# Optimization experiments

Measured on AMD Instinct MI355X. Metric: run time of the kernel, lower is better.

## Reference

```python
import jax, jax.numpy as jnp
import numpy as np

GROUPS = 32
EPS = 1e-5


def _group_norm(x, w, b):
    B, C, H, W = x.shape
    xr = x.reshape(B, GROUPS, C // GROUPS, H, W)
    mean = xr.mean(axis=(2, 3, 4), keepdims=True)
    var = xr.var(axis=(2, 3, 4), keepdims=True)
    xn = ((xr - mean) * jax.lax.rsqrt(var + EPS)).reshape(B, C, H, W)
    return xn * w[None, :, None, None] + b[None, :, None, None]


def _conv1x1(w, b, x):
    # 1x1 conv == per-pixel channel matmul
    return jnp.einsum('oc,bchw->bohw', w, x) + b[None, :, None, None]


def setup_inputs() -> dict:
    key = jax.random.key(0)
    ks = jax.random.split(key, 6)
    C = 512
    s = 1.0 / np.sqrt(C)  # kaiming-uniform-ish scale for 1x1 convs
    return {
        'x': jax.random.normal(ks[0], (4, C, 64, 64), jnp.float32),
        'gn_w': jnp.ones((C,), jnp.float32),
        'gn_b': jnp.zeros((C,), jnp.float32),
        'qw': jax.random.normal(ks[1], (C, C), jnp.float32) * s,
        'qb': jnp.zeros((C,), jnp.float32),
        'kw': jax.random.normal(ks[2], (C, C), jnp.float32) * s,
        'kb': jnp.zeros((C,), jnp.float32),
        'vw': jax.random.normal(ks[3], (C, C), jnp.float32) * s,
        'vb': jnp.zeros((C,), jnp.float32),
        'pw': jax.random.normal(ks[4], (C, C), jnp.float32) * s,
        'pb': jnp.zeros((C,), jnp.float32),
    }


def reference(x, gn_w, gn_b, qw, qb, kw, kb, vw, vb, pw, pb):
    B, C, H, W = x.shape
    h_ = _group_norm(x, gn_w, gn_b)
    q = _conv1x1(qw, qb, h_).reshape(B, C, H * W)
    k = _conv1x1(kw, kb, h_).reshape(B, C, H * W)
    v = _conv1x1(vw, vb, h_).reshape(B, C, H * W)
    # scores [B, HW(query), HW(key)]
    scores = jnp.einsum('bcq,bck->bqk', q, k) * (C ** -0.5)
    attn = jax.nn.softmax(scores, axis=-1)
    out = jnp.einsum('bqk,bdk->bdq', attn, v).reshape(B, C, H, W)
    return x + _conv1x1(pw, pb, out)
```

## Files before the change

kernel.cpp:

```cpp
#include <hip/hip_runtime.h>

#define DEV __device__ __forceinline__

typedef __attribute__((ext_vector_type(8))) short short8;
typedef __attribute__((ext_vector_type(4))) float floatx4;
typedef __attribute__((ext_vector_type(4))) int i32x4;
typedef __attribute__((ext_vector_type(2))) long longx2;

DEV unsigned short f2bs(float x) {
    unsigned u = __float_as_uint(x);
    unsigned r = (u + 0x7fffu + ((u >> 16) & 1u)) >> 16;
    return (unsigned short)r;
}

DEV unsigned char f2fp8(float x) {
#if __has_builtin(__builtin_amdgcn_cvt_pk_fp8_f32)
    int pk = __builtin_amdgcn_cvt_pk_fp8_f32(x, 0.f, 0, false);
    return (unsigned char)(pk & 0xff);
#else
    unsigned u = __float_as_uint(x);
    unsigned s = (u >> 24) & 0x80;
    unsigned a = u & 0x7fffffff;
    unsigned um = a + 0x7ffffu + ((a >> 20) & 1u);
    unsigned r = (a >= 0x3c800000u) ? ((um >> 20) - 0x3C0u) : 0u;
    return (unsigned char)(r | s);
#endif
}

DEV unsigned pack_fp8x4(float v0, float v1, float v2, float v3) {
#if __has_builtin(__builtin_amdgcn_cvt_pk_fp8_f32)
    unsigned pk = (unsigned)__builtin_amdgcn_cvt_pk_fp8_f32(v0, v1, 0, false);
    pk = (unsigned)__builtin_amdgcn_cvt_pk_fp8_f32(v2, v3, (int)pk, true);
    return pk;
#else
    return (unsigned)f2fp8(v0) | ((unsigned)f2fp8(v1) << 8) |
           ((unsigned)f2fp8(v2) << 16) | ((unsigned)f2fp8(v3) << 24);
#endif
}

DEV unsigned pack_i8x4(float v0, float v1, float v2, float v3) {
    unsigned b0 = (unsigned)((int)rintf(v0)) & 255u;
    unsigned b1 = (unsigned)((int)rintf(v1)) & 255u;
    unsigned b2 = (unsigned)((int)rintf(v2)) & 255u;
    unsigned b3 = (unsigned)((int)rintf(v3)) & 255u;
    return b0 | (b1 << 8) | (b2 << 16) | (b3 << 24);
}

DEV void syncfull() {
    asm volatile("s_waitcnt vmcnt(0) lgkmcnt(0)" ::: "memory");
    __builtin_amdgcn_sched_barrier(0);
    __builtin_amdgcn_s_barrier();
    __builtin_amdgcn_sched_barrier(0);
}

__global__ void pre_kernel(const float* __restrict__ x,
                           const float* __restrict__ qw, const float* __restrict__ kw,
                           const float* __restrict__ vw, const float* __restrict__ pw,
                           const float* __restrict__ qb, const float* __restrict__ kb,
                           unsigned short* __restrict__ wqkb, unsigned short* __restrict__ wvb,
                           unsigned short* __restrict__ wpb,
                           float* __restrict__ biasqk,
                           float* __restrict__ stats) {
    int b = blockIdx.x, tid = threadIdx.x;
    if (b < 768) {
        const float* src = (b < 256) ? qw : (b < 512) ? kw : vw;
        unsigned short* dst = (b < 256) ? wqkb : (b < 512) ? (wqkb + 262144) : wvb;
        int off = (b & 255) * 256 + tid;
        float4 v = ((const float4*)src)[off];
        ushort4 o;
        o.x = f2bs(v.x); o.y = f2bs(v.y); o.z = f2bs(v.z); o.w = f2bs(v.w);
        ((ushort4*)dst)[off] = o;
    } else if (b < 1024) {
        int off = (b - 768) * 256 + tid;
        int row = off >> 7, c4 = (off & 127) * 4;
        float4 v = ((const float4*)pw)[off];
        float vv[4] = {v.x, v.y, v.z, v.w};
#pragma unroll
        for (int e = 0; e < 4; ++e) {
            int c = c4 + e;
            int j = (c >> 4) & 3, lc = c & 15;
            int cp = (c & ~63) | (lc * 4 + j);
            wpb[row * 512 + cp] = f2bs(vv[e]);
        }
    } else if (b == 1024) {
        biasqk[tid]       = qb[tid];
        biasqk[256 + tid] = qb[256 + tid];
        biasqk[512 + tid] = kb[tid];
        biasqk[768 + tid] = kb[256 + tid];
    } else {
        int bg = b - 1025;
        const float4* p = (const float4*)(x + (size_t)bg * 65536);
        float s = 0.f, ss = 0.f;
        for (int i = tid; i < 16384; i += 256) {
            float4 v = p[i];
            s += v.x + v.y + v.z + v.w;
            ss += v.x * v.x + v.y * v.y + v.z * v.z + v.w * v.w;
        }
        for (int off = 32; off; off >>= 1) { s += __shfl_down(s, off); ss += __shfl_down(ss, off); }
        __shared__ float rs[4], rss[4];
        int wave = tid >> 6, lane = tid & 63;
        if (lane == 0) { rs[wave] = s; rss[wave] = ss; }
        __syncthreads();
        if (tid == 0) {
            float S = rs[0] + rs[1] + rs[2] + rs[3];
            float SS = rss[0] + rss[1] + rss[2] + rss[3];
            float mean = S * (1.f / 65536.f);
            float var = SS * (1.f / 65536.f) - mean * mean;
            stats[bg * 2] = mean;
            stats[bg * 2 + 1] = rsqrtf(var + 1e-5f);
        }
    }
}

__global__ void gn_apply_kernel(const float* __restrict__ x, const float* __restrict__ stats,
                                const float* __restrict__ gw, const float* __restrict__ gb,
                                unsigned short* __restrict__ ht) {
    __shared__ __align__(16) unsigned short t[64][72];
    int b = blockIdx.z, c0 = blockIdx.y * 64, p0 = blockIdx.x * 64;
    int tid = threadIdx.x;
    const float* xb = x + ((size_t)b * 512 + c0) * 4096 + p0;
#pragma unroll
    for (int pass = 0; pass < 4; ++pass) {
        int cl = pass * 16 + (tid >> 4);
        int pq = (tid & 15) * 4;
        float4 v = *(const float4*)(xb + (size_t)cl * 4096 + pq);
        int c = c0 + cl, g = c >> 4;
        float mean = stats[(b * 32 + g) * 2], rstd = stats[(b * 32 + g) * 2 + 1];
        float sw = gw[c] * rstd;
        float sb = gb[c] - mean * sw;
        t[pq + 0][cl] = f2bs(v.x * sw + sb);
        t[pq + 1][cl] = f2bs(v.y * sw + sb);
        t[pq + 2][cl] = f2bs(v.z * sw + sb);
        t[pq + 3][cl] = f2bs(v.w * sw + sb);
    }
    __syncthreads();
    unsigned short* hb = ht + ((size_t)b * 4096 + p0) * 512 + c0;
#pragma unroll
    for (int pass = 0; pass < 2; ++pass) {
        int pl = pass * 32 + (tid >> 3);
        int c8 = (tid & 7) * 8;
        *(uint4*)(hb + (size_t)pl * 512 + c8) = *(const uint4*)&t[pl][c8];
    }
}

__global__ void gemm_qkv(const unsigned short* __restrict__ h_t, long long sP,
                         const unsigned short* __restrict__ wqkb,
                         const unsigned short* __restrict__ wvb,
                         char* __restrict__ q_i8, char* __restrict__ k_i8,
                         char* __restrict__ v_f8,
                         const float* __restrict__ biasqk, const float* __restrict__ vb,
                         float qs) {
    __shared__ __align__(16) unsigned short lA[128 * 64];
    __shared__ __align__(16) unsigned short lB[128 * 64];
    const int tid = threadIdx.x;
    const int wave = tid >> 6, lane = tid & 63;
    const int flat = blockIdx.x;
    const bool isqk = flat < 1024;
    int m0, n0, bz;
    const unsigned short *Ab, *Bb;
    if (isqk) {
        m0 = ((flat >> 3) & 31) * 128;
        n0 = (flat & 7) * 128;
        bz = flat >> 8;
        Ab = h_t + (size_t)bz * sP;
        Bb = wqkb;
    } else {
        const int g = flat - 1024;
        m0 = ((g >> 5) & 3) * 128;
        n0 = (g & 31) * 128;
        bz = g >> 7;
        Ab = wvb;
        Bb = h_t + (size_t)bz * sP;
    }

    floatx4 acc[4][4];
#pragma unroll
    for (int i = 0; i < 4; i++)
#pragma unroll
        for (int j = 0; j < 4; j++) acc[i][j] = (floatx4){0.f, 0.f, 0.f, 0.f};

    const int wm = (wave >> 1) * 64, wn = (wave & 1) * 64;
    const int quad = lane >> 4;
    const int lc = lane & 15;
    const int lc7 = lc & 7;

    for (int kt = 0; kt < 8; ++kt) {
        const int kbase = kt * 64;
#pragma unroll
        for (int c = 0; c < 4; ++c) {
            int d = c * 256 + tid;
            int r = d >> 3;
            int kc = (d & 7) ^ (r & 7);
            const unsigned short* ga = Ab + (size_t)(m0 + r) * 512 + kbase + kc * 8;
            const unsigned short* gb = Bb + (size_t)(n0 + r) * 512 + kbase + kc * 8;
            __builtin_amdgcn_global_load_lds(
                (const __attribute__((address_space(1))) void*)ga,
                (__attribute__((address_space(3))) void*)&lA[(size_t)(c * 256 + wave * 64) * 8], 16, 0, 0);
            __builtin_amdgcn_global_load_lds(
                (const __attribute__((address_space(1))) void*)gb,
                (__attribute__((address_space(3))) void*)&lB[(size_t)(c * 256 + wave * 64) * 8], 16, 0, 0);
        }
        __syncthreads();
#pragma unroll
        for (int kk = 0; kk < 2; ++kk) {
            const int swz = ((kk * 4 + quad) ^ lc7) * 8;
            short8 af[4], bf[4];
#pragma unroll
            for (int i = 0; i < 4; i++)
                af[i] = *(const short8*)&lA[(size_t)(wm + i * 16 + lc) * 64 + swz];
#pragma unroll
            for (int j = 0; j < 4; j++)
                bf[j] = *(const short8*)&lB[(size_t)(wn + j * 16 + lc) * 64 + swz];
#pragma unroll
            for (int i = 0; i < 4; i++)
#pragma unroll
                for (int j = 0; j < 4; j++)
                    acc[i][j] = __builtin_amdgcn_mfma_f32_16x16x32_bf16(af[i], bf[j], acc[i][j], 0, 0, 0);
        }
        __syncthreads();
    }

    const int rowb = quad * 4;
    if (isqk) {
#pragma unroll
        for (int i = 0; i < 4; i++) {
#pragma unroll
            for (int r = 0; r < 4; r++) {
                const int m = m0 + wm + i * 16 + rowb + r;
                float q[4];
#pragma unroll
                for (int j = 0; j < 4; j++) {
                    const int n = n0 + wn + j * 16 + lc;
                    q[j] = fminf(fmaxf((acc[i][j][r] + biasqk[n]) * qs, -127.f), 127.f);
                }
                const int col64 = n0 + wn;
                char* outp = (col64 < 512) ? q_i8 : k_i8;
                size_t idx = (size_t)bz * sP + (size_t)m * 512 +
                             (col64 - ((col64 < 512) ? 0 : 512)) + lc * 4;
                *(unsigned*)(outp + idx) = pack_i8x4(q[0], q[1], q[2], q[3]);
            }
        }
    } else {
#pragma unroll
        for (int i = 0; i < 4; i++) {
#pragma unroll
            for (int r = 0; r < 4; r++) {
                const int m = m0 + wm + i * 16 + rowb + r;
                const float bm = vb[m];
                float q[4];
#pragma unroll
                for (int j = 0; j < 4; j++)
                    q[j] = fminf(fmaxf(acc[i][j][r] + bm, -448.f), 448.f);
                size_t idx = (size_t)bz * sP + (size_t)m * 4096 + n0 + wn + lc * 4;
                *(unsigned*)(v_f8 + idx) = pack_fp8x4(q[0], q[1], q[2], q[3]);
            }
        }
    }
}

__global__ void gemm_proj(const unsigned short* __restrict__ A,
                          const unsigned short* __restrict__ B, long long sBb,
                          float* __restrict__ Cv, long long sCb,
                          const float* __restrict__ bias,
                          const float* __restrict__ resid, long long sRb,
                          const float* __restrict__ rsum,
                          int M, int N, int K) {
    __shared__ __align__(16) unsigned short lA[128 * 64];
    __shared__ __align__(16) unsigned short lB[128 * 64];
    const int tid = threadIdx.x;
    const int wave = tid >> 6, lane = tid & 63;
    const int m0 = blockIdx.y * 128, n0 = blockIdx.x * 128, bz = blockIdx.z;
    const unsigned short* Ab = A;
    const unsigned short* Bb = B + (size_t)bz * sBb;

    floatx4 acc[4][4];
#pragma unroll
    for (int i = 0; i < 4; i++)
#pragma unroll
        for (int j = 0; j < 4; j++) acc[i][j] = (floatx4){0.f, 0.f, 0.f, 0.f};

    const int wm = (wave >> 1) * 64, wn = (wave & 1) * 64;
    const int quad = lane >> 4;
    const int lc = lane & 15;
    const int lc7 = lc & 7;

    const int nk = K >> 6;
    for (int kt = 0; kt < nk; ++kt) {
        const int kbase = kt * 64;
#pragma unroll
        for (int c = 0; c < 4; ++c) {
            int d = c * 256 + tid;
            int r = d >> 3;
            int kc = (d & 7) ^ (r & 7);
            const unsigned short* ga = Ab + (size_t)(m0 + r) * 512 + ((kbase & 511) + kc * 8);
            const unsigned short* gb = Bb + (size_t)(n0 + r) * 1024 + kbase + kc * 8;
            __builtin_amdgcn_global_load_lds(
                (const __attribute__((address_space(1))) void*)ga,
                (__attribute__((address_space(3))) void*)&lA[(size_t)(c * 256 + wave * 64) * 8], 16, 0, 0);
            __builtin_amdgcn_global_load_lds(
                (const __attribute__((address_space(1))) void*)gb,
                (__attribute__((address_space(3))) void*)&lB[(size_t)(c * 256 + wave * 64) * 8], 16, 0, 0);
        }
        __syncthreads();
#pragma unroll
        for (int kk = 0; kk < 2; ++kk) {
            const int swz = ((kk * 4 + quad) ^ lc7) * 8;
            short8 af[4], bf[4];
#pragma unroll
            for (int i = 0; i < 4; i++)
                af[i] = *(const short8*)&lA[(size_t)(wm + i * 16 + lc) * 64 + swz];
#pragma unroll
            for (int j = 0; j < 4; j++)
                bf[j] = *(const short8*)&lB[(size_t)(wn + j * 16 + lc) * 64 + swz];
#pragma unroll
            for (int i = 0; i < 4; i++)
#pragma unroll
                for (int j = 0; j < 4; j++)
                    acc[i][j] = __builtin_amdgcn_mfma_f32_16x16x32_bf16(af[i], bf[j], acc[i][j], 0, 0, 0);
        }
        __syncthreads();
    }

    float rsinv[4];
#pragma unroll
    for (int j = 0; j < 4; j++) {
        const int n = n0 + wn + j * 16 + lc;
        rsinv[j] = 1.f / (rsum[(size_t)bz * 4096 + n] + rsum[(size_t)(4 + bz) * 4096 + n]);
    }

    const int rowb = quad * 4;
#pragma unroll
    for (int i = 0; i < 4; i++) {
#pragma unroll
        for (int r = 0; r < 4; r++) {
            const int m = m0 + wm + i * 16 + rowb + r;
            const float bm = bias[m];
#pragma unroll
            for (int j = 0; j < 4; j++) {
                const int n = n0 + wn + j * 16 + lc;
                size_t idx = (size_t)bz * sCb + (size_t)m * N + n;
                Cv[idx] = acc[i][j][r] * rsinv[j] + bm + resid[(size_t)bz * sRb + (size_t)m * N + n];
            }
        }
    }
}

__global__ __launch_bounds__(512, 2) void attn_fused(
    const char* __restrict__ Qg, const char* __restrict__ Kg,
    const char* __restrict__ Vg,
    unsigned short* __restrict__ Ou, long long sOb,
    float* __restrict__ rsum, float scale2) {
    __shared__ __align__(16) char Ql[512 * 128];
    __shared__ __align__(16) char Kl[256 * 128];
    __shared__ __align__(16) char Vl[256 * 128];
    __shared__ __align__(16) char Pl[128 * 80];
    const int tid = threadIdx.x;
    const int wave = tid >> 6, lane = tid & 63;
    const int quad = lane >> 4, lc = lane & 15;
    const int lc7 = lc & 7;
    const int id = blockIdx.x;
    const int xcd = id & 7, qi = id >> 3;
    const int bz = xcd >> 1, split = xcd & 1;
    const int q0 = qi * 128;
    const int kvbase = split * 2048;
    const int NIT = 32;

    const char* Qb = Qg + ((size_t)bz * 4096 + q0) * 512;
    const char* Kb = Kg + ((size_t)bz * 4096 + kvbase) * 512;
    const char* Vb = Vg + (size_t)bz * 2097152 + kvbase;

    const int wq = wave * 16;
    const int mO = (wave >> 2) * 64, nO = (wave & 3) * 128;

    auto stageQ = [&]() {
#pragma unroll
        for (int c = 0; c < 8; ++c) {
            int f = c * 512 + tid;
            int rr = f >> 3, cs = f & 7;
            int qq = rr & 127, chq = rr >> 7;
            int s = cs ^ (qq & 7);
            __builtin_amdgcn_global_load_lds(
                (const __attribute__((address_space(1))) void*)(Qb + (size_t)qq * 512 + chq * 128 + s * 16),
                (__attribute__((address_space(3))) void*)(Ql + (size_t)f * 16), 16, 0, 0);
        }
    };
    auto stageK = [&](int t) {
#pragma unroll
        for (int c = 0; c < 4; ++c) {
            int f = c * 512 + tid;
            int rr = f >> 3, cs = f & 7;
            int kv = rr & 63, chq = rr >> 6;
            int s = cs ^ (kv & 7);
            __builtin_amdgcn_global_load_lds(
                (const __attribute__((address_space(1))) void*)(Kb + (size_t)(t * 64 + kv) * 512 + chq * 128 + s * 16),
                (__attribute__((address_space(3))) void*)(Kl + (size_t)f * 16), 16, 0, 0);
        }
    };
    auto stageV = [&](int t) {
#pragma unroll
        for (int c = 0; c < 4; ++c) {
            int f = c * 512 + tid;
            int rr = f >> 3, cs = f & 7;
            int cp = cs ^ (rr & 7);
            int d = rr + ((cp >> 2) << 8);
            int gq = cp & 3;
            __builtin_amdgcn_global_load_lds(
                (const __attribute__((address_space(1))) void*)(Vb + (size_t)d * 4096 + t * 64 + gq * 16),
                (__attribute__((address_space(3))) void*)(Vl + (size_t)f * 16), 16, 0, 0);
        }
    };

    floatx4 acco[4][8];
#pragma unroll
    for (int i = 0; i < 4; ++i)
#pragma unroll
        for (int j = 0; j < 8; ++j) acco[i][j] = (floatx4){0.f, 0.f, 0.f, 0.f};
    float rs = 0.f;

    stageQ();
    stageK(0);
    stageV(0);
    syncfull();

    const int q = wq + lc;
    const int q7 = q & 7;

    for (int t = 0; t < NIT; ++t) {
        if (t > 0) stageV(t);
        i32x4 accs[4];
#pragma unroll
        for (int ki = 0; ki < 4; ++ki) accs[ki] = (i32x4){0, 0, 0, 0};
#pragma unroll
        for (int ks = 0; ks < 8; ++ks) {
            const int g = ks * 4 + quad;
            const int gh = g >> 3, gl = g & 7;
            i32x4 bfrag = *(const i32x4*)&Ql[(size_t)(gh * 128 + q) * 128 + ((gl ^ q7) << 4)];
#pragma unroll
            for (int ki = 0; ki < 4; ++ki) {
                const int ar = ki * 16 + lc;
                i32x4 afrag = *(const i32x4*)&Kl[(size_t)(gh * 64 + ar) * 128 + ((gl ^ lc7) << 4)];
                accs[ki] = __builtin_amdgcn_mfma_i32_16x16x64_i8(afrag, bfrag, accs[ki], 0, 0, 0);
            }
        }
        float e[4][4];
#pragma unroll
        for (int ki = 0; ki < 4; ++ki)
#pragma unroll
            for (int r = 0; r < 4; ++r) {
                e[ki][r] = fminf(exp2f(fmaf((float)accs[ki][r], scale2, -2.0f)), 448.f);
                rs += e[ki][r];
            }
        {
            unsigned w0 = pack_fp8x4(e[0][0], e[1][0], e[2][0], e[3][0]);
            unsigned w1 = pack_fp8x4(e[0][1], e[1][1], e[2][1], e[3][1]);
            unsigned w2 = pack_fp8x4(e[0][2], e[1][2], e[2][2], e[3][2]);
            unsigned w3 = pack_fp8x4(e[0][3], e[1][3], e[2][3], e[3][3]);
            uint2 s0; s0.x = w0; s0.y = w1;
            uint2 s1; s1.x = w2; s1.y = w3;
            *(uint2*)&Pl[(size_t)q * 80 + quad * 16 + 0] = s0;
            *(uint2*)&Pl[(size_t)q * 80 + quad * 16 + 8] = s1;
        }
        syncfull();

        if (t + 1 < NIT) stageK(t + 1);
        {
            longx2 pv[4], vv[8];
#pragma unroll
            for (int i = 0; i < 4; ++i) {
                const int row = mO + i * 16 + lc;
                pv[i] = *(const longx2*)&Pl[(size_t)row * 80 + quad * 16];
            }
#pragma unroll
            for (int j = 0; j < 8; ++j) {
                const int row = nO + j * 16 + lc;
                const int r8 = row & 255, hi = row >> 8;
                vv[j] = *(const longx2*)&Vl[(size_t)r8 * 128 + (((hi << 2) + quad) ^ lc7) * 16];
            }
#pragma unroll
            for (int i = 0; i < 4; ++i)
#pragma unroll
                for (int j = 0; j < 8; ++j)
                    acco[i][j] = __builtin_amdgcn_mfma_f32_16x16x32_fp8_fp8(pv[i][0], vv[j][0], acco[i][j], 0, 0, 0);
#pragma unroll
            for (int i = 0; i < 4; ++i)
#pragma unroll
                for (int j = 0; j < 8; ++j)
                    acco[i][j] = __builtin_amdgcn_mfma_f32_16x16x32_fp8_fp8(pv[i][1], vv[j][1], acco[i][j], 0, 0, 0);
        }
        syncfull();
    }

    rs += __shfl_xor(rs, 16);
    rs += __shfl_xor(rs, 32);
    if (quad == 0) rsum[((size_t)(split * 4 + bz)) * 4096 + q0 + q] = rs;

#pragma unroll
    for (int i = 0; i < 4; ++i) {
#pragma unroll
        for (int r = 0; r < 4; ++r) {
            const int m = q0 + mO + i * 16 + quad * 4 + r;
            unsigned short h[8];
#pragma unroll
            for (int j = 0; j < 8; ++j) h[j] = f2bs(acco[i][j][r]);
            unsigned short* base = Ou + (size_t)bz * sOb + (size_t)m * 1024 + split * 512 + nO;
            uint2 u0, u1;
            u0.x = (unsigned)h[0] | ((unsigned)h[1] << 16);
            u0.y = (unsigned)h[2] | ((unsigned)h[3] << 16);
            u1.x = (unsigned)h[4] | ((unsigned)h[5] << 16);
            u1.y = (unsigned)h[6] | ((unsigned)h[7] << 16);
            *(uint2*)(base + lc * 4) = u0;
            *(uint2*)(base + 64 + lc * 4) = u1;
        }
    }
}

extern "C" void kernel_launch(void* const* d_in, const int* in_sizes, int n_in,
                              void* d_out, int out_size, void* d_ws, size_t ws_size,
                              hipStream_t stream) {
    (void)in_sizes; (void)n_in; (void)out_size; (void)ws_size;
    const float* x   = (const float*)d_in[0];
    const float* gnw = (const float*)d_in[1];
    const float* gnb = (const float*)d_in[2];
    const float* qw  = (const float*)d_in[3];
    const float* qb  = (const float*)d_in[4];
    const float* kw  = (const float*)d_in[5];
    const float* kb  = (const float*)d_in[6];
    const float* vw  = (const float*)d_in[7];
    const float* vb  = (const float*)d_in[8];
    const float* pw  = (const float*)d_in[9];
    const float* pb  = (const float*)d_in[10];
    float* out = (float*)d_out;

    char* ws = (char*)d_ws;
    unsigned short* h_t = (unsigned short*)(ws);
    char* q_i8 = (char*)(ws + (16ull << 20));
    char* k_i8 = (char*)(ws + (32ull << 20));
    char* v_f8 = (char*)(ws + (48ull << 20));
    unsigned short* wqkb = (unsigned short*)(ws + (64ull << 20));
    unsigned short* wvb = (unsigned short*)(ws + (65ull << 20));
    unsigned short* wpb = wvb + 262144;
    float* stats  = (float*)(ws + (66ull << 20));
    float* biasqk = (float*)(ws + (66ull << 20) + 8192);
    float* rowsum = (float*)(ws + (66ull << 20) + 65536);
    unsigned short* o_un = (unsigned short*)(ws + (72ull << 20));

    const long long sP  = 2097152;
    const long long sOb = 4194304;
    const float QS = 16.f;
    const float SC = 0.044194173824159216f / (QS * QS);
    const float LOG2E = 1.4426950408889634f;

    pre_kernel<<<1153, 256, 0, stream>>>(x, qw, kw, vw, pw, qb, kb, wqkb, wvb, wpb,
                                         biasqk, stats);
    gn_apply_kernel<<<dim3(64, 8, 4), 256, 0, stream>>>(x, stats, gnw, gnb, h_t);
    gemm_qkv<<<1536, 256, 0, stream>>>(h_t, sP, wqkb, wvb, q_i8, k_i8, v_f8, biasqk, vb, QS);
    attn_fused<<<dim3(256), 512, 0, stream>>>(q_i8, k_i8, v_f8, o_un, sOb, rowsum,
                                              SC * LOG2E);
    gemm_proj<<<dim3(32, 4, 4), 256, 0, stream>>>(wpb, o_un, sOb, out, sP, pb, x, sP,
                                                  rowsum, 512, 4096, 1024);
}
```

Baseline: 291.3 us.

## Switch attention PV product to 32x32x64 scaled fp8 MFMA with new LDS layouts

Replaces the 16x16x32 fp8 MFMAs in the P·V stage with the gfx950 mfma_scale_f32_32x32x64_f8f6f4 instruction, using unit scales. This requires rearranging the P tile and V tile in LDS (new swizzles, pair-row packing) and changing the output projection weight permutation to match the new output column order. The goal is to cut MFMA instruction count and LDS fragment reads per FLOP. It risks higher register pressure from the 16-wide accumulators, and correctness depends on the permutation in the epilogue and in the pw weights matching.

```diff
diff --git a/kernel.cpp b/kernel.cpp
--- a/kernel.cpp
+++ b/kernel.cpp
@@ -4,7 +4,9 @@
 
 typedef __attribute__((ext_vector_type(8))) short short8;
 typedef __attribute__((ext_vector_type(4))) float floatx4;
+typedef __attribute__((ext_vector_type(16))) float floatx16;
 typedef __attribute__((ext_vector_type(4))) int i32x4;
+typedef __attribute__((ext_vector_type(8))) int i32x8;
 typedef __attribute__((ext_vector_type(2))) long longx2;
 
 DEV unsigned short f2bs(float x) {
@@ -78,8 +80,7 @@
 #pragma unroll
         for (int e = 0; e < 4; ++e) {
             int c = c4 + e;
-            int j = (c >> 4) & 3, lc = c & 15;
-            int cp = (c & ~63) | (lc * 4 + j);
+            int cp = (c & ~63) | (((c & 31) << 1) | ((c >> 5) & 1));
             wpb[row * 512 + cp] = f2bs(vv[e]);
         }
     } else if (b == 1024) {
@@ -353,11 +354,12 @@
     __shared__ __align__(16) char Ql[512 * 128];
     __shared__ __align__(16) char Kl[256 * 128];
     __shared__ __align__(16) char Vl[256 * 128];
-    __shared__ __align__(16) char Pl[128 * 80];
+    __shared__ __align__(16) char Pl[64 * 128];
     const int tid = threadIdx.x;
     const int wave = tid >> 6, lane = tid & 63;
     const int quad = lane >> 4, lc = lane & 15;
     const int lc7 = lc & 7;
+    const int l31 = lane & 31, lh = lane >> 5;
     const int id = blockIdx.x;
     const int xcd = id & 7, qi = id >> 3;
     const int bz = xcd >> 1, split = xcd & 1;
@@ -400,21 +402,22 @@
 #pragma unroll
         for (int c = 0; c < 4; ++c) {
             int f = c * 512 + tid;
-            int rr = f >> 3, cs = f & 7;
-            int cp = cs ^ (rr & 7);
-            int d = rr + ((cp >> 2) << 8);
-            int gq = cp & 3;
+            int u = (f & 7) ^ ((f >> 3) & 7);
+            int d = ((f >> 3) << 1) | (u >> 2);
+            int gq = u & 3;
             __builtin_amdgcn_global_load_lds(
                 (const __attribute__((address_space(1))) void*)(Vb + (size_t)d * 4096 + t * 64 + gq * 16),
                 (__attribute__((address_space(3))) void*)(Vl + (size_t)f * 16), 16, 0, 0);
         }
     };
 
-    floatx4 acco[4][8];
-#pragma unroll
-    for (int i = 0; i < 4; ++i)
-#pragma unroll
-        for (int j = 0; j < 8; ++j) acco[i][j] = (floatx4){0.f, 0.f, 0.f, 0.f};
+    floatx16 acco[2][4];
+#pragma unroll
+    for (int i = 0; i < 2; ++i)
+#pragma unroll
+        for (int j = 0; j < 4; ++j)
+#pragma unroll
+            for (int r = 0; r < 16; ++r) acco[i][j][r] = 0.f;
     float rs = 0.f;
 
     stageQ();
@@ -455,37 +458,40 @@
             unsigned w1 = pack_fp8x4(e[0][1], e[1][1], e[2][1], e[3][1]);
             unsigned w2 = pack_fp8x4(e[0][2], e[1][2], e[2][2], e[3][2]);
             unsigned w3 = pack_fp8x4(e[0][3], e[1][3], e[2][3], e[3][3]);
-            uint2 s0; s0.x = w0; s0.y = w1;
-            uint2 s1; s1.x = w2; s1.y = w3;
-            *(uint2*)&Pl[(size_t)q * 80 + quad * 16 + 0] = s0;
-            *(uint2*)&Pl[(size_t)q * 80 + quad * 16 + 8] = s1;
+            const int L = q >> 1;
+            const int sl = ((((q & 1) << 2) | quad) ^ (L & 7));
+            *(i32x4*)&Pl[(size_t)L * 128 + (sl << 4)] = (i32x4){(int)w0, (int)w1, (int)w2, (int)w3};
         }
         syncfull();
 
         if (t + 1 < NIT) stageK(t + 1);
         {
-            longx2 pv[4], vv[8];
-#pragma unroll
-            for (int i = 0; i < 4; ++i) {
-                const int row = mO + i * 16 + lc;
-                pv[i] = *(const longx2*)&Pl[(size_t)row * 80 + quad * 16];
-            }
-#pragma unroll
-            for (int j = 0; j < 8; ++j) {
-                const int row = nO + j * 16 + lc;
-                const int r8 = row & 255, hi = row >> 8;
-                vv[j] = *(const longx2*)&Vl[(size_t)r8 * 128 + (((hi << 2) + quad) ^ lc7) * 16];
-            }
-#pragma unroll
-            for (int i = 0; i < 4; ++i)
-#pragma unroll
-                for (int j = 0; j < 8; ++j)
-                    acco[i][j] = __builtin_amdgcn_mfma_f32_16x16x32_fp8_fp8(pv[i][0], vv[j][0], acco[i][j], 0, 0, 0);
-#pragma unroll
-            for (int i = 0; i < 4; ++i)
-#pragma unroll
-                for (int j = 0; j < 8; ++j)
-                    acco[i][j] = __builtin_amdgcn_mfma_f32_16x16x32_fp8_fp8(pv[i][1], vv[j][1], acco[i][j], 0, 0, 0);
+            i32x8 pa[2], vv[4];
+#pragma unroll
+            for (int i = 0; i < 2; ++i) {
+                const int r_ = mO + i * 32 + l31;
+                const int L = r_ >> 1;
+                const int sb = ((r_ & 1) << 2) | (lh << 1);
+                i32x4 lo = *(const i32x4*)&Pl[(size_t)L * 128 + ((sb ^ (L & 7)) << 4)];
+                i32x4 hi = *(const i32x4*)&Pl[(size_t)L * 128 + (((sb | 1) ^ (L & 7)) << 4)];
+                pa[i] = __builtin_shufflevector(lo, hi, 0, 1, 2, 3, 4, 5, 6, 7);
+            }
+#pragma unroll
+            for (int j = 0; j < 4; ++j) {
+                const int r_ = nO + j * 32 + l31;
+                const int L = r_ >> 1;
+                const int sb = ((r_ & 1) << 2) | (lh << 1);
+                i32x4 lo = *(const i32x4*)&Vl[(size_t)L * 128 + ((sb ^ (L & 7)) << 4)];
+                i32x4 hi = *(const i32x4*)&Vl[(size_t)L * 128 + (((sb | 1) ^ (L & 7)) << 4)];
+                vv[j] = __builtin_shufflevector(lo, hi, 0, 1, 2, 3, 4, 5, 6, 7);
+            }
+#pragma unroll
+            for (int i = 0; i < 2; ++i)
+#pragma unroll
+                for (int j = 0; j < 4; ++j)
+                    acco[i][j] = __builtin_amdgcn_mfma_scale_f32_32x32x64_f8f6f4(
+                        pa[i], vv[j], acco[i][j], 0, 0,
+                        0, 0x7f7f7f7f, 0, 0x7f7f7f7f);
         }
         syncfull();
     }
@@ -495,21 +501,15 @@
     if (quad == 0) rsum[((size_t)(split * 4 + bz)) * 4096 + q0 + q] = rs;
 
 #pragma unroll
-    for (int i = 0; i < 4; ++i) {
-#pragma unroll
-        for (int r = 0; r < 4; ++r) {
-            const int m = q0 + mO + i * 16 + quad * 4 + r;
-            unsigned short h[8];
-#pragma unroll
-            for (int j = 0; j < 8; ++j) h[j] = f2bs(acco[i][j][r]);
+    for (int i = 0; i < 2; ++i) {
+#pragma unroll
+        for (int reg = 0; reg < 16; ++reg) {
+            const int m = q0 + mO + i * 32 + (reg & 3) + 8 * (reg >> 2) + 4 * lh;
+            unsigned u01 = (unsigned)f2bs(acco[i][0][reg]) | ((unsigned)f2bs(acco[i][1][reg]) << 16);
+            unsigned u23 = (unsigned)f2bs(acco[i][2][reg]) | ((unsigned)f2bs(acco[i][3][reg]) << 16);
             unsigned short* base = Ou + (size_t)bz * sOb + (size_t)m * 1024 + split * 512 + nO;
-            uint2 u0, u1;
-            u0.x = (unsigned)h[0] | ((unsigned)h[1] << 16);
-            u0.y = (unsigned)h[2] | ((unsigned)h[3] << 16);
-            u1.x = (unsigned)h[4] | ((unsigned)h[5] << 16);
-            u1.y = (unsigned)h[6] | ((unsigned)h[7] << 16);
-            *(uint2*)(base + lc * 4) = u0;
-            *(uint2*)(base + 64 + lc * 4) = u1;
+            *(unsigned*)(base + l31 * 2) = u01;
+            *(unsigned*)(base + 64 + l31 * 2) = u23;
         }
     }
 }
```

New measurement: 278.8 us. 4.3% less time.
